# Kernel optimization log

Hardware: AMD Instinct MI355X
Metric: run time of the kernel (lower is better)

The kernel has to match this reference:

```python
import jax, jax.numpy as jnp
import numpy as np

HIDDEN = 1024


def setup_inputs() -> dict:
    key = jax.random.key(0)
    ks = jax.random.split(key, 9)
    B, S, Kq, H = 16, 4096, 64, HIDDEN
    scale = 1.0 / np.sqrt(H)
    return {
        "queries": jax.random.normal(ks[0], (B, Kq, H), jnp.float32),
        "keys": jax.random.normal(ks[1], (B, S, H), jnp.float32),
        "values": jax.random.normal(ks[2], (B, S, H), jnp.float32),
        "Wq": jax.random.normal(ks[3], (H, H), jnp.float32) * scale,
        "bq": jax.random.normal(ks[4], (H,), jnp.float32) * 0.02,
        "Wk": jax.random.normal(ks[5], (H, H), jnp.float32) * scale,
        "bk": jax.random.normal(ks[6], (H,), jnp.float32) * 0.02,
        "Wv": jax.random.normal(ks[7], (H, H), jnp.float32) * scale,
        "bv": jax.random.normal(ks[8], (H,), jnp.float32) * 0.02,
    }


def reference(queries, keys, values, Wq, bq, Wk, bk, Wv, bv):
    H = Wq.shape[0]
    scaling = jax.lax.rsqrt(jnp.asarray(H, queries.dtype))
    # torch Linear: x @ W^T + b
    q = queries @ Wq.T + bq            # (B, Kq, H)
    k = keys @ Wk.T + bk               # (B, S, H)
    v = values @ Wv.T + bv             # (B, S, H)
    # scores: k @ q^T -> (B, S, Kq), softmax over seq_len axis (dim=1)
    scores = jnp.einsum('bsh,bqh->bsq', k, q) * scaling
    attention_weights = jax.nn.softmax(scores, axis=1)
    # context: attn^T @ v -> (B, Kq, H)
    context = jnp.einsum('bsq,bsh->bqh', attention_weights, v)
    return context, attention_weights
```

## Files before the change

kernel.cpp:

```cpp
#include <hip/hip_runtime.h>
#include <hip/hip_bf16.h>

#define H 1024
#define SEQ 4096
#define BQ 64
#define NB 16

typedef float f32x4 __attribute__((ext_vector_type(4)));
typedef __bf16 bf16x8 __attribute__((ext_vector_type(8)));

__device__ __forceinline__ void split_bf16(const float* x, bf16x8& hi, bf16x8& lo)
{
    #pragma unroll
    for (int i = 0; i < 8; ++i) {
        float v = x[i];
        __bf16 h = (__bf16)v;
        hi[i] = h;
        lo[i] = (__bf16)(v - (float)h);
    }
}

__device__ __forceinline__ void gload_lds16(const void* g, void* lds)
{
    __builtin_amdgcn_global_load_lds(
        (const __attribute__((address_space(1))) void*)g,
        (__attribute__((address_space(3))) void*)lds, 16, 0, 0);
}

template<bool CVEC>
__global__ __launch_bounds__(512)
void gemm_bt_512(const float* __restrict__ A, const float* __restrict__ Bm,
                 const float* __restrict__ bias, float* __restrict__ C,
                 float scale, const float* __restrict__ bk,
                 float* __restrict__ cvec, float cscale)
{
    const int m0 = blockIdx.x * 64;
    const int n0 = blockIdx.y * 64;
    const int t   = threadIdx.x;
    const int w   = t >> 6;
    const int wm  = w & 3;
    const int kh  = w >> 2;
    const int l   = t & 63;
    const int row = l & 15;
    const int kg  = l >> 4;

    const float* ap = A + (size_t)(m0 + wm * 16 + row) * H + kh * 512 + kg * 8;
    const float* bp = Bm + (size_t)(n0 + row) * H + kh * 512 + kg * 8;

    f32x4 acc[4] = {};
    for (int k0 = 0; k0 < 512; k0 += 32) {
        float a8[8];
        *reinterpret_cast<float4*>(&a8[0]) = *reinterpret_cast<const float4*>(ap + k0);
        *reinterpret_cast<float4*>(&a8[4]) = *reinterpret_cast<const float4*>(ap + k0 + 4);
        bf16x8 ahi, alo;
        split_bf16(a8, ahi, alo);
        #pragma unroll
        for (int j = 0; j < 4; ++j) {
            float b8[8];
            const float* bjp = bp + (size_t)j * 16 * H + k0;
            *reinterpret_cast<float4*>(&b8[0]) = *reinterpret_cast<const float4*>(bjp);
            *reinterpret_cast<float4*>(&b8[4]) = *reinterpret_cast<const float4*>(bjp + 4);
            bf16x8 bhi, blo;
            split_bf16(b8, bhi, blo);
            acc[j] = __builtin_amdgcn_mfma_f32_16x16x32_bf16(ahi, bhi, acc[j], 0, 0, 0);
            acc[j] = __builtin_amdgcn_mfma_f32_16x16x32_bf16(ahi, blo, acc[j], 0, 0, 0);
            acc[j] = __builtin_amdgcn_mfma_f32_16x16x32_bf16(alo, bhi, acc[j], 0, 0, 0);
        }
    }

    __shared__ f32x4 red[4][4][64];
    if (kh == 1) {
        #pragma unroll
        for (int j = 0; j < 4; ++j) red[wm][j][l] = acc[j];
    }
    __syncthreads();
    if (kh == 0) {
        float p[4] = {0.f, 0.f, 0.f, 0.f};
        #pragma unroll
        for (int j = 0; j < 4; ++j) {
            f32x4 s = acc[j] + red[wm][j][l];
            int n = n0 + j * 16 + row;
            float bb = bias ? bias[n] : 0.f;
            float bkv = CVEC ? bk[n] : 0.f;
            #pragma unroll
            for (int r = 0; r < 4; ++r) {
                int m = m0 + wm * 16 + kg * 4 + r;
                float o = s[r] * scale + bb;
                C[(size_t)m * H + n] = o;
                if (CVEC) p[r] += o * bkv;
            }
        }
        if (CVEC) {
            #pragma unroll
            for (int r = 0; r < 4; ++r) {
                #pragma unroll
                for (int off = 1; off < 16; off <<= 1)
                    p[r] += __shfl_xor(p[r], off);
            }
            if (row == 0) {
                #pragma unroll
                for (int r = 0; r < 4; ++r)
                    atomicAdd(&cvec[m0 + wm * 16 + kg * 4 + r], p[r] * cscale);
            }
        }
    }
}

__global__ __launch_bounds__(512)
void ngemm_direct(const float* __restrict__ A, const float* __restrict__ Wk,
                  __bf16* __restrict__ Nhi, __bf16* __restrict__ Nlo, float scale)
{
    const int m0 = blockIdx.x * 64;
    const int n0 = blockIdx.y * 64;
    const int t   = threadIdx.x;
    const int w   = t >> 6;
    const int wm  = w & 3;
    const int kh  = w >> 2;
    const int l   = t & 63;
    const int row = l & 15;
    const int kg  = l >> 4;

    const float* ap = A + (size_t)(m0 + wm * 16 + row) * H + kh * 512 + kg * 8;
    const float* bp = Wk + (size_t)(kh * 512 + kg * 8) * H + n0 + row;

    f32x4 acc[4] = {};
    for (int k0 = 0; k0 < 512; k0 += 32) {
        float a8[8];
        *reinterpret_cast<float4*>(&a8[0]) = *reinterpret_cast<const float4*>(ap + k0);
        *reinterpret_cast<float4*>(&a8[4]) = *reinterpret_cast<const float4*>(ap + k0 + 4);
        bf16x8 ahi, alo;
        split_bf16(a8, ahi, alo);
        #pragma unroll
        for (int j = 0; j < 4; ++j) {
            float b8[8];
            #pragma unroll
            for (int e = 0; e < 8; ++e)
                b8[e] = bp[(size_t)(k0 + e) * H + j * 16];
            bf16x8 bhi, blo;
            split_bf16(b8, bhi, blo);
            acc[j] = __builtin_amdgcn_mfma_f32_16x16x32_bf16(ahi, bhi, acc[j], 0, 0, 0);
            acc[j] = __builtin_amdgcn_mfma_f32_16x16x32_bf16(ahi, blo, acc[j], 0, 0, 0);
            acc[j] = __builtin_amdgcn_mfma_f32_16x16x32_bf16(alo, bhi, acc[j], 0, 0, 0);
        }
    }

    __shared__ f32x4 red[4][4][64];
    if (kh == 1) {
        #pragma unroll
        for (int j = 0; j < 4; ++j) red[wm][j][l] = acc[j];
    }
    __syncthreads();
    if (kh == 0) {
        #pragma unroll
        for (int j = 0; j < 4; ++j) {
            f32x4 s = acc[j] + red[wm][j][l];
            int n = n0 + j * 16 + row;
            #pragma unroll
            for (int r = 0; r < 4; ++r) {
                int m = m0 + wm * 16 + kg * 4 + r;
                float v = s[r] * scale;
                __bf16 hi = (__bf16)v;
                Nhi[(size_t)m * H + n] = hi;
                Nlo[(size_t)m * H + n] = (__bf16)(v - (float)hi);
            }
        }
    }
}

__global__ __launch_bounds__(512, 4)
void scores_mfma(const float* __restrict__ keys,
                 const __bf16* __restrict__ Nhi, const __bf16* __restrict__ Nlo,
                 const float* __restrict__ cvec, float* __restrict__ scores,
                 float* __restrict__ pmax, float* __restrict__ psum)
{
    const int id = blockIdx.x;
    const int x  = id & 7;
    const int m  = id >> 3;
    const int b  = 2 * x + (m >> 5);
    const int ch = m & 31;
    const int s0 = ch * 128;

    const int t   = threadIdx.x;
    const int w   = t >> 6;
    const int l   = t & 63;
    const int row = l & 15;
    const int kg  = l >> 4;

    __shared__ __bf16 nshH[2][64][8][8];
    __shared__ __bf16 nshL[2][64][8][8];
    __shared__ float redm[8][64];

    const float* ka = keys + ((size_t)b * SEQ + s0 + w * 16 + row) * H + kg * 8;
    const __bf16* nhb = Nhi + (size_t)b * BQ * H;
    const __bf16* nlb = Nlo + (size_t)b * BQ * H;

    const int sqi = t >> 3;
    const int skb = t & 7;
    const int ssl = skb ^ (sqi & 7);

    float4 kr[2][4];
    bf16x8 nh[2], nl[2];
    #pragma unroll
    for (int ii = 0; ii < 2; ++ii) {
        kr[0][2 * ii + 0] = *reinterpret_cast<const float4*>(ka + ii * 32);
        kr[0][2 * ii + 1] = *reinterpret_cast<const float4*>(ka + ii * 32 + 4);
    }
    {
        size_t go = (size_t)sqi * H + skb * 8;
        nh[0] = *reinterpret_cast<const bf16x8*>(nhb + go);
        nl[0] = *reinterpret_cast<const bf16x8*>(nlb + go);
    }

    f32x4 acc[4] = {};
    #pragma unroll
    for (int c = 0; c < 16; ++c) {
        const int buf = c & 1;
        *reinterpret_cast<bf16x8*>(&nshH[buf][sqi][ssl][0]) = nh[buf];
        *reinterpret_cast<bf16x8*>(&nshL[buf][sqi][ssl][0]) = nl[buf];
        __syncthreads();
        if (c < 15) {
            const int kc = (c + 1) * 64;
            #pragma unroll
            for (int ii = 0; ii < 2; ++ii) {
                kr[buf ^ 1][2 * ii + 0] = *reinterpret_cast<const float4*>(ka + kc + ii * 32);
                kr[buf ^ 1][2 * ii + 1] = *reinterpret_cast<const float4*>(ka + kc + ii * 32 + 4);
            }
            size_t go = (size_t)sqi * H + kc + skb * 8;
            nh[buf ^ 1] = *reinterpret_cast<const bf16x8*>(nhb + go);
            nl[buf ^ 1] = *reinterpret_cast<const bf16x8*>(nlb + go);
        }
        #pragma unroll
        for (int ii = 0; ii < 2; ++ii) {
            float a8[8];
            *reinterpret_cast<float4*>(&a8[0]) = kr[buf][2 * ii + 0];
            *reinterpret_cast<float4*>(&a8[4]) = kr[buf][2 * ii + 1];
            bf16x8 ahi, alo;
            split_bf16(a8, ahi, alo);
            const int kb = ii * 4 + kg;
            const int slot = kb ^ (row & 7);
            #pragma unroll
            for (int j = 0; j < 4; ++j) {
                const int qi = j * 16 + row;
                bf16x8 bhi = *reinterpret_cast<const bf16x8*>(&nshH[buf][qi][slot][0]);
                bf16x8 blo = *reinterpret_cast<const bf16x8*>(&nshL[buf][qi][slot][0]);
                acc[j] = __builtin_amdgcn_mfma_f32_16x16x32_bf16(ahi, bhi, acc[j], 0, 0, 0);
                acc[j] = __builtin_amdgcn_mfma_f32_16x16x32_bf16(ahi, blo, acc[j], 0, 0, 0);
                acc[j] = __builtin_amdgcn_mfma_f32_16x16x32_bf16(alo, bhi, acc[j], 0, 0, 0);
            }
        }
    }

    #pragma unroll
    for (int j = 0; j < 4; ++j) {
        int qi = j * 16 + row;
        float cv = cvec[b * BQ + qi];
        #pragma unroll
        for (int r = 0; r < 4; ++r) {
            acc[j][r] += cv;
            int s = s0 + w * 16 + kg * 4 + r;
            scores[((size_t)b * SEQ + s) * BQ + qi] = acc[j][r];
        }
    }
    float mj[4];
    #pragma unroll
    for (int j = 0; j < 4; ++j) {
        float mm = fmaxf(fmaxf(acc[j][0], acc[j][1]), fmaxf(acc[j][2], acc[j][3]));
        mm = fmaxf(mm, __shfl_xor(mm, 16));
        mm = fmaxf(mm, __shfl_xor(mm, 32));
        mj[j] = mm;
    }
    __syncthreads();
    if (kg == 0) {
        #pragma unroll
        for (int j = 0; j < 4; ++j) redm[w][j * 16 + row] = mj[j];
    }
    __syncthreads();
    float Mj[4];
    #pragma unroll
    for (int j = 0; j < 4; ++j) {
        const int qi = j * 16 + row;
        float M = redm[0][qi];
        #pragma unroll
        for (int ww = 1; ww < 8; ++ww) M = fmaxf(M, redm[ww][qi]);
        Mj[j] = M;
    }
    float sj[4];
    #pragma unroll
    for (int j = 0; j < 4; ++j) {
        float s = 0.f;
        #pragma unroll
        for (int r = 0; r < 4; ++r) s += __expf(acc[j][r] - Mj[j]);
        s += __shfl_xor(s, 16);
        s += __shfl_xor(s, 32);
        sj[j] = s;
    }
    __syncthreads();
    if (kg == 0) {
        #pragma unroll
        for (int j = 0; j < 4; ++j) redm[w][j * 16 + row] = sj[j];
    }
    __syncthreads();
    if (w == 0 && kg == 0) {
        #pragma unroll
        for (int j = 0; j < 4; ++j) {
            const int qi = j * 16 + row;
            float ss = 0.f;
            #pragma unroll
            for (int ww = 0; ww < 8; ++ww) ss += redm[ww][qi];
            pmax[((size_t)b * 32 + ch) * 64 + qi] = Mj[j];
            psum[((size_t)b * 32 + ch) * 64 + qi] = ss;
        }
    }
}

__global__ __launch_bounds__(256)
void sm_norm(float* __restrict__ attn, const float* __restrict__ pmax,
             const float* __restrict__ psum, __hip_bfloat16* __restrict__ abfT)
{
    __shared__ float tile[64][133];
    const int b  = blockIdx.y;
    const int ch = blockIdx.x;
    const int t  = threadIdx.x;
    const int qi = t & 63;
    const int g  = t >> 6;

    float M = -1e30f;
    #pragma unroll 4
    for (int c = 0; c < 32; ++c)
        M = fmaxf(M, pmax[((size_t)b * 32 + c) * 64 + qi]);
    float ssum = 0.f;
    #pragma unroll 4
    for (int c = 0; c < 32; ++c)
        ssum += psum[((size_t)b * 32 + c) * 64 + qi] *
                __expf(pmax[((size_t)b * 32 + c) * 64 + qi] - M);
    const float inv = 1.f / ssum;

    float* sb = attn + ((size_t)b * SEQ + ch * 128) * BQ;
    #pragma unroll 8
    for (int i = 0; i < 32; ++i) {
        int sl = g + i * 4;
        size_t idx = (size_t)sl * BQ + qi;
        float w = __expf(sb[idx] - M) * inv;
        sb[idx] = w;
        tile[qi][sl] = w;
    }
    __syncthreads();
    const int qo = t >> 2;
    const int c  = (t & 3) * 32;
    __hip_bfloat16* dst = abfT + ((size_t)(b * BQ + qo)) * SEQ + ch * 128 + c;
    #pragma unroll
    for (int v = 0; v < 4; ++v) {
        bf16x8 w8;
        #pragma unroll
        for (int e = 0; e < 8; ++e)
            w8[e] = (__bf16)tile[qo][c + v * 8 + e];
        *reinterpret_cast<bf16x8*>(dst + v * 8) = w8;
    }
}

template<int SC>
__global__ __launch_bounds__(256)
void tmat_mfma(const __hip_bfloat16* __restrict__ abfT,
               const float* __restrict__ values,
               float* __restrict__ Tpart)
{
    constexpr int schunk = SEQ / SC;
    constexpr int nk = schunk / 32;

    const int i  = blockIdx.x;
    const int h0 = ((i >> 3) & 7) * 128;
    const int g  = (i & 7) + 8 * (i >> 6);
    const int b  = g / SC;
    const int sc = g % SC;

    const int w   = threadIdx.x >> 6;
    const int l   = threadIdx.x & 63;
    const int row = l & 15;
    const int kg  = l >> 4;
    const int sbase = sc * schunk;

    __shared__ float vlds[3][32][128];
    __shared__ __hip_bfloat16 alds[3][64][32];

    const __hip_bfloat16* ab = abfT + (size_t)b * BQ * SEQ + sbase;
    const float* vb = values + ((size_t)b * SEQ + sbase) * H + h0;

    #define VSTAGE(buf, c)                                                     \
        {                                                                      \
            _Pragma("unroll")                                                  \
            for (int ii = 0; ii < 4; ++ii) {                                   \
                int elem = w * 1024 + ii * 256 + l * 4;                        \
                int k    = elem >> 7;                                          \
                int cc   = elem & 127;                                         \
                int csw  = cc ^ ((k >> 3) << 4);                               \
                const float* src = vb + (size_t)((c) * 32 + k) * H + csw;      \
                gload_lds16(src, (void*)(&vlds[buf][0][0] + w * 1024 + ii * 256)); \
            }                                                                  \
        }
    #define ASTAGE(buf, c)                                                     \
        {                                                                      \
            int aqi = w * 16 + (l >> 2);                                       \
            const __hip_bfloat16* srcA =                                       \
                ab + (size_t)aqi * SEQ + (c) * 32 + (l & 3) * 8;               \
            gload_lds16(srcA, (void*)(&alds[buf][0][0] + w * 512));            \
        }

    f32x4 acc[4][2] = {};
    ASTAGE(0, 0); VSTAGE(0, 0);
    ASTAGE(1, 1); VSTAGE(1, 1);

    for (int ks = 0; ks < nk; ++ks) {
        const int buf = ks % 3;
        if (ks + 2 < nk) {
            const int nb2 = (ks + 2) % 3;
            ASTAGE(nb2, ks + 2); VSTAGE(nb2, ks + 2);
            asm volatile("s_waitcnt vmcnt(10)" ::: "memory");
        } else if (ks + 1 < nk) {
            asm volatile("s_waitcnt vmcnt(5)" ::: "memory");
        } else {
            asm volatile("s_waitcnt vmcnt(0)" ::: "memory");
        }
        __builtin_amdgcn_sched_barrier(0);
        __builtin_amdgcn_s_barrier();
        __builtin_amdgcn_sched_barrier(0);

        __builtin_amdgcn_s_setprio(1);
        bf16x8 a[4];
        #pragma unroll
        for (int q = 0; q < 4; ++q)
            a[q] = *reinterpret_cast<const bf16x8*>(&alds[buf][q * 16 + row][kg * 8]);
        #pragma unroll
        for (int j = 0; j < 2; ++j) {
            const int col = (w * 32 + j * 16 + row) ^ (kg << 4);
            float b8[8];
            #pragma unroll
            for (int e = 0; e < 8; ++e)
                b8[e] = vlds[buf][kg * 8 + e][col];
            bf16x8 bhi, blo;
            split_bf16(b8, bhi, blo);
            #pragma unroll
            for (int q = 0; q < 4; ++q) {
                acc[q][j] = __builtin_amdgcn_mfma_f32_16x16x32_bf16(a[q], bhi, acc[q][j], 0, 0, 0);
                acc[q][j] = __builtin_amdgcn_mfma_f32_16x16x32_bf16(a[q], blo, acc[q][j], 0, 0, 0);
            }
        }
        __builtin_amdgcn_s_setprio(0);
        __builtin_amdgcn_sched_barrier(0);
        __builtin_amdgcn_s_barrier();
        __builtin_amdgcn_sched_barrier(0);
    }
    #undef VSTAGE
    #undef ASTAGE

    float* tp = Tpart + ((size_t)sc * NB + b) * BQ * H;
    #pragma unroll
    for (int q = 0; q < 4; ++q) {
        #pragma unroll
        for (int j = 0; j < 2; ++j) {
            int h = h0 + w * 32 + j * 16 + row;
            #pragma unroll
            for (int r = 0; r < 4; ++r) {
                int qi = q * 16 + kg * 4 + r;
                tp[(size_t)qi * H + h] = acc[q][j][r];
            }
        }
    }
}

template<int SC>
__global__ __launch_bounds__(256)
void tsum_kernel(float* __restrict__ Tpart)
{
    const size_t stride = (size_t)NB * BQ * H;
    size_t i = ((size_t)blockIdx.x * 256 + threadIdx.x) * 4;
    f32x4 s = *reinterpret_cast<const f32x4*>(Tpart + i);
    #pragma unroll
    for (int p = 1; p < SC; ++p)
        s += *reinterpret_cast<const f32x4*>(Tpart + p * stride + i);
    *reinterpret_cast<f32x4*>(Tpart + i) = s;
}

extern "C" void kernel_launch(void* const* d_in, const int* in_sizes, int n_in,
                              void* d_out, int out_size, void* d_ws, size_t ws_size,
                              hipStream_t stream)
{
    const float* queries = (const float*)d_in[0];
    const float* keys    = (const float*)d_in[1];
    const float* values  = (const float*)d_in[2];
    const float* Wq = (const float*)d_in[3];
    const float* bq = (const float*)d_in[4];
    const float* Wk = (const float*)d_in[5];
    const float* bk = (const float*)d_in[6];
    const float* Wv = (const float*)d_in[7];
    const float* bv = (const float*)d_in[8];

    float* out     = (float*)d_out;
    float* context = out;
    float* attn    = out + (size_t)NB * BQ * H;

    const int SC = (ws_size >= (41ull << 20)) ? 8 : 2;

    char* ws = (char*)d_ws;
    float* q     = (float*)ws;
    __bf16* Nhi  = (__bf16*)(ws + (8ull << 20));
    __bf16* Nlo  = (__bf16*)(ws + (10ull << 20));
    float* Tpart = (float*)ws;
    __hip_bfloat16* abfT = (__hip_bfloat16*)(ws + (size_t)SC * (4ull << 20));
    char* smalls = ws + (size_t)SC * (4ull << 20) + (8ull << 20);
    float* cvec  = (float*)smalls;
    float* pmax  = (float*)(smalls + (128u << 10));
    float* psum  = (float*)(smalls + (512u << 10));

    const float scale = 0.03125f;

    hipMemsetAsync(cvec, 0, (size_t)NB * BQ * sizeof(float), stream);
    gemm_bt_512<true><<<dim3(16, 16), 512, 0, stream>>>(
        queries, Wq, bq, q, 1.0f, bk, cvec, scale);
    ngemm_direct<<<dim3(16, 16), 512, 0, stream>>>(q, Wk, Nhi, Nlo, scale);
    scores_mfma<<<512, 512, 0, stream>>>(keys, Nhi, Nlo, cvec, attn, pmax, psum);
    sm_norm<<<dim3(32, NB), 256, 0, stream>>>(attn, pmax, psum, abfT);
    if (SC == 8) tmat_mfma<8><<<8 * NB * 8, 256, 0, stream>>>(abfT, values, Tpart);
    else         tmat_mfma<2><<<8 * NB * 2, 256, 0, stream>>>(abfT, values, Tpart);
    if (SC == 8) tsum_kernel<8><<<1024, 256, 0, stream>>>(Tpart);
    else         tsum_kernel<2><<<1024, 256, 0, stream>>>(Tpart);
    gemm_bt_512<false><<<dim3(16, 16), 512, 0, stream>>>(
        Tpart, Wv, bv, context, 1.0f, nullptr, nullptr, 0.f);
}
```

Before: 277.1 us.

## Stage keys and Nhi/Nlo via direct global-to-LDS loads in triple-buffered pipeline

Rewrites the scores_mfma main loop so keys and the hi/lo bf16 query projections are copied into swizzled LDS with global_load_lds. The copies run in a three-stage ring with explicit vmcnt waits, s_barrier and setprio around the MFMA block. The loop now steps through K in chunks of 32 instead of 64. The aim is to hide global load latency and cut register staging and VGPR pressure. The launch bounds drop to 2 blocks per SM, and the extra barriers per step add synchronisation overhead.

```diff
diff --git a/kernel.cpp b/kernel.cpp
--- a/kernel.cpp
+++ b/kernel.cpp
@@ -167,7 +167,7 @@
     }
 }
 
-__global__ __launch_bounds__(512, 4)
+__global__ __launch_bounds__(512, 2)
 void scores_mfma(const float* __restrict__ keys,
                  const __bf16* __restrict__ Nhi, const __bf16* __restrict__ Nlo,
                  const float* __restrict__ cvec, float* __restrict__ scores,
@@ -186,69 +186,86 @@
     const int row = l & 15;
     const int kg  = l >> 4;
 
-    __shared__ __bf16 nshH[2][64][8][8];
-    __shared__ __bf16 nshL[2][64][8][8];
-    __shared__ float redm[8][64];
-
-    const float* ka = keys + ((size_t)b * SEQ + s0 + w * 16 + row) * H + kg * 8;
-    const __bf16* nhb = Nhi + (size_t)b * BQ * H;
-    const __bf16* nlb = Nlo + (size_t)b * BQ * H;
-
-    const int sqi = t >> 3;
-    const int skb = t & 7;
-    const int ssl = skb ^ (sqi & 7);
-
-    float4 kr[2][4];
-    bf16x8 nh[2], nl[2];
-    #pragma unroll
-    for (int ii = 0; ii < 2; ++ii) {
-        kr[0][2 * ii + 0] = *reinterpret_cast<const float4*>(ka + ii * 32);
-        kr[0][2 * ii + 1] = *reinterpret_cast<const float4*>(ka + ii * 32 + 4);
-    }
-    {
-        size_t go = (size_t)sqi * H + skb * 8;
-        nh[0] = *reinterpret_cast<const bf16x8*>(nhb + go);
-        nl[0] = *reinterpret_cast<const bf16x8*>(nlb + go);
-    }
+    __shared__ float  klds[3][128][4][8];
+    __shared__ __bf16 nhlds[3][64][4][8];
+    __shared__ __bf16 nllds[3][64][4][8];
+    __shared__ float  redm[8][64];
+
+    const float*  kbase = keys + ((size_t)b * SEQ + s0) * H;
+    const __bf16* nhb   = Nhi + (size_t)b * BQ * H;
+    const __bf16* nlb   = Nlo + (size_t)b * BQ * H;
+
+    #define KSTAGE(buf, c)                                                     \
+        {                                                                      \
+            _Pragma("unroll")                                                  \
+            for (int ii = 0; ii < 2; ++ii) {                                   \
+                int d  = w * 512 + ii * 256 + l * 4;                           \
+                int ss = d >> 5;                                               \
+                int sb = (d >> 3) & 3;                                         \
+                int e0 = d & 7;                                                \
+                const float* src = kbase + (size_t)ss * H + (c) * 32 +         \
+                                   ((sb ^ (ss & 3)) << 3) + e0;                \
+                gload_lds16(src, (void*)(&klds[buf][0][0][0] + w * 512 + ii * 256)); \
+            }                                                                  \
+        }
+    #define NSTAGE(buf, c)                                                     \
+        {                                                                      \
+            int d   = (w & 3) * 512 + l * 8;                                   \
+            int qi_ = d >> 5;                                                  \
+            int nb_ = (d >> 3) & 3;                                            \
+            const __bf16* srcN = ((w < 4) ? nhb : nlb) + (size_t)qi_ * H +     \
+                                 (c) * 32 + ((nb_ ^ (qi_ & 3)) << 3);          \
+            __bf16* dstN = ((w < 4) ? &nhlds[buf][0][0][0]                     \
+                                    : &nllds[buf][0][0][0]) + (w & 3) * 512;   \
+            gload_lds16(srcN, (void*)dstN);                                    \
+        }
 
     f32x4 acc[4] = {};
-    #pragma unroll
-    for (int c = 0; c < 16; ++c) {
-        const int buf = c & 1;
-        *reinterpret_cast<bf16x8*>(&nshH[buf][sqi][ssl][0]) = nh[buf];
-        *reinterpret_cast<bf16x8*>(&nshL[buf][sqi][ssl][0]) = nl[buf];
-        __syncthreads();
-        if (c < 15) {
-            const int kc = (c + 1) * 64;
-            #pragma unroll
-            for (int ii = 0; ii < 2; ++ii) {
-                kr[buf ^ 1][2 * ii + 0] = *reinterpret_cast<const float4*>(ka + kc + ii * 32);
-                kr[buf ^ 1][2 * ii + 1] = *reinterpret_cast<const float4*>(ka + kc + ii * 32 + 4);
-            }
-            size_t go = (size_t)sqi * H + kc + skb * 8;
-            nh[buf ^ 1] = *reinterpret_cast<const bf16x8*>(nhb + go);
-            nl[buf ^ 1] = *reinterpret_cast<const bf16x8*>(nlb + go);
-        }
-        #pragma unroll
-        for (int ii = 0; ii < 2; ++ii) {
-            float a8[8];
-            *reinterpret_cast<float4*>(&a8[0]) = kr[buf][2 * ii + 0];
-            *reinterpret_cast<float4*>(&a8[4]) = kr[buf][2 * ii + 1];
-            bf16x8 ahi, alo;
-            split_bf16(a8, ahi, alo);
-            const int kb = ii * 4 + kg;
-            const int slot = kb ^ (row & 7);
-            #pragma unroll
-            for (int j = 0; j < 4; ++j) {
-                const int qi = j * 16 + row;
-                bf16x8 bhi = *reinterpret_cast<const bf16x8*>(&nshH[buf][qi][slot][0]);
-                bf16x8 blo = *reinterpret_cast<const bf16x8*>(&nshL[buf][qi][slot][0]);
-                acc[j] = __builtin_amdgcn_mfma_f32_16x16x32_bf16(ahi, bhi, acc[j], 0, 0, 0);
-                acc[j] = __builtin_amdgcn_mfma_f32_16x16x32_bf16(ahi, blo, acc[j], 0, 0, 0);
-                acc[j] = __builtin_amdgcn_mfma_f32_16x16x32_bf16(alo, bhi, acc[j], 0, 0, 0);
-            }
-        }
-    }
+    KSTAGE(0, 0); NSTAGE(0, 0);
+    KSTAGE(1, 1); NSTAGE(1, 1);
+
+    const int sw    = w * 16 + row;
+    const int aslot = kg ^ (row & 3);
+
+    for (int ks = 0; ks < 32; ++ks) {
+        const int buf = ks % 3;
+        if (ks + 2 < 32) {
+            const int nb2 = (ks + 2) % 3;
+            KSTAGE(nb2, ks + 2); NSTAGE(nb2, ks + 2);
+            asm volatile("s_waitcnt vmcnt(6)" ::: "memory");
+        } else if (ks + 1 < 32) {
+            asm volatile("s_waitcnt vmcnt(3)" ::: "memory");
+        } else {
+            asm volatile("s_waitcnt vmcnt(0)" ::: "memory");
+        }
+        __builtin_amdgcn_sched_barrier(0);
+        __builtin_amdgcn_s_barrier();
+        __builtin_amdgcn_sched_barrier(0);
+
+        __builtin_amdgcn_s_setprio(1);
+        float a8[8];
+        *reinterpret_cast<float4*>(&a8[0]) =
+            *reinterpret_cast<const float4*>(&klds[buf][sw][aslot][0]);
+        *reinterpret_cast<float4*>(&a8[4]) =
+            *reinterpret_cast<const float4*>(&klds[buf][sw][aslot][4]);
+        bf16x8 ahi, alo;
+        split_bf16(a8, ahi, alo);
+        #pragma unroll
+        for (int j = 0; j < 4; ++j) {
+            const int qi = j * 16 + row;
+            bf16x8 bhi = *reinterpret_cast<const bf16x8*>(&nhlds[buf][qi][aslot][0]);
+            bf16x8 blo = *reinterpret_cast<const bf16x8*>(&nllds[buf][qi][aslot][0]);
+            acc[j] = __builtin_amdgcn_mfma_f32_16x16x32_bf16(ahi, bhi, acc[j], 0, 0, 0);
+            acc[j] = __builtin_amdgcn_mfma_f32_16x16x32_bf16(ahi, blo, acc[j], 0, 0, 0);
+            acc[j] = __builtin_amdgcn_mfma_f32_16x16x32_bf16(alo, bhi, acc[j], 0, 0, 0);
+        }
+        __builtin_amdgcn_s_setprio(0);
+        __builtin_amdgcn_sched_barrier(0);
+        __builtin_amdgcn_s_barrier();
+        __builtin_amdgcn_sched_barrier(0);
+    }
+    #undef KSTAGE
+    #undef NSTAGE
 
     #pragma unroll
     for (int j = 0; j < 4; ++j) {
```

Result: no change. 277.4 us (+0.1%).
